# Kernel optimization log

Hardware: AMD Instinct MI355X
Metric: run time of the kernel (lower is better)

Reference implementation:

```python
import jax, jax.numpy as jnp
import numpy as np

B, S, H = 2, 1024, 4096
NH, NKV, HD = 32, 8, 128
THETA = 500000.0
EPS = 1e-6


def _ste(x, q):
    # straight-through estimator: forward q, gradient of identity
    return x + jax.lax.stop_gradient(q - x)


def weight_quant(w):
    # BitNet b1.58 ternary weight quantization (per-tensor mean-abs scale)
    scale = 1.0 / jnp.clip(jnp.mean(jnp.abs(w)), 1e-5)
    wq = jnp.clip(jnp.round(w * scale), -1.0, 1.0) / scale
    return _ste(w, wq)


def act_quant(x):
    # per-token int8 absmax activation quantization
    scale = 127.0 / jnp.clip(jnp.max(jnp.abs(x), axis=-1, keepdims=True), 1e-5)
    xq = jnp.clip(jnp.round(x * scale), -128.0, 127.0) / scale
    return _ste(x, xq)


def bitlinear(x, w):
    # torch Linear convention: w is (out, in)
    return act_quant(x) @ weight_quant(w).T


def rmsnorm(x, w):
    return x * jax.lax.rsqrt(jnp.mean(x * x, axis=-1, keepdims=True) + EPS) * w


def rope(x, cos, sin):
    # x: (b, s, h, hd); pairs are interleaved (even, odd) like view_as_complex
    x2 = x.reshape(*x.shape[:-1], HD // 2, 2)
    a, b = x2[..., 0], x2[..., 1]
    c = cos[None, :, None, :]
    s = sin[None, :, None, :]
    out = jnp.stack([a * c - b * s, a * s + b * c], axis=-1)
    return out.reshape(x.shape)


def setup_inputs() -> dict:
    key = jax.random.key(0)
    ks = jax.random.split(key, 6)
    hidden_states = jax.random.normal(ks[0], (B, S, H), dtype=jnp.float32)
    causal = jnp.tril(jnp.ones((S, S), dtype=bool))
    attention_mask = jnp.where(causal, 0.0, -1e9).astype(jnp.float32)[None, None]
    w_q = jax.random.normal(ks[1], (NH * HD, H), dtype=jnp.float32) * 0.02
    w_k = jax.random.normal(ks[2], (NKV * HD, H), dtype=jnp.float32) * 0.02
    w_v = jax.random.normal(ks[3], (NKV * HD, H), dtype=jnp.float32) * 0.02
    w_o = jax.random.normal(ks[4], (H, NH * HD), dtype=jnp.float32) * 0.02
    subln_w = jnp.ones((NH * HD,), dtype=jnp.float32)
    return {"hidden_states": hidden_states, "attention_mask": attention_mask,
            "w_q": w_q, "w_k": w_k, "w_v": w_v, "w_o": w_o, "subln_w": subln_w}


def reference(hidden_states, attention_mask, w_q, w_k, w_v, w_o, subln_w):
    b, s, _ = hidden_states.shape
    # RoPE tables (precomputed buffer in torch, constant here)
    inv_freq = 1.0 / (THETA ** (jnp.arange(0, HD, 2, dtype=jnp.float32) / HD))
    freqs = jnp.arange(s, dtype=jnp.float32)[:, None] * inv_freq[None, :]  # (s, hd/2)
    cos, sin = jnp.cos(freqs), jnp.sin(freqs)

    q = bitlinear(hidden_states, w_q).reshape(b, s, NH, HD)
    k = bitlinear(hidden_states, w_k).reshape(b, s, NKV, HD)
    v = bitlinear(hidden_states, w_v).reshape(b, s, NKV, HD)

    q = rope(q, cos, sin)
    k = rope(k, cos, sin)

    # GQA: repeat kv heads
    n_rep = NH // NKV
    k = jnp.repeat(k, n_rep, axis=2)  # (b, s, NH, hd)
    v = jnp.repeat(v, n_rep, axis=2)

    scale = 1.0 / np.sqrt(HD)
    scores = jnp.einsum('bqhd,bkhd->bhqk', q, k) * scale
    scores = scores + attention_mask
    attn = jax.nn.softmax(scores.astype(jnp.float32), axis=-1).astype(q.dtype)
    out = jnp.einsum('bhqk,bkhd->bqhd', attn, v).reshape(b, s, NH * HD)

    out = rmsnorm(out, subln_w)  # SubLN before output projection
    out = bitlinear(out, w_o)
    return out
```

## Files before the change

### kernel.cpp

```cpp
#include <hip/hip_runtime.h>
#include <hip/hip_bf16.h>
#include <cstdint>

typedef unsigned short u16;
typedef __bf16 bf16x8 __attribute__((ext_vector_type(8)));
typedef float f32x4 __attribute__((ext_vector_type(4)));
typedef int i32x4 __attribute__((ext_vector_type(4)));

#define SEQ 1024
#define HID 4096
#define NHQ 32
#define NKVH 8
#define HDIM 128
#define NB 2
#define NROWS (NB*SEQ)

static __device__ __forceinline__ u16 f2bf(float x) {
  __hip_bfloat16 h = __float2bfloat16(x);
  return *reinterpret_cast<u16*>(&h);
}

static __device__ __forceinline__ void gload16(const void* g, void* l) {
  __builtin_amdgcn_global_load_lds((__attribute__((address_space(1))) void*)(void*)g,
                                   (__attribute__((address_space(3))) void*)l, 16, 0, 0);
}

static __device__ __forceinline__ int pack4i8(float a, float b, float c, float d,
                                              float s, float lo, float hi) {
  int x0 = (int)fminf(fmaxf(rintf(a*s), lo), hi);
  int x1 = (int)fminf(fmaxf(rintf(b*s), lo), hi);
  int x2 = (int)fminf(fmaxf(rintf(c*s), lo), hi);
  int x3 = (int)fminf(fmaxf(rintf(d*s), lo), hi);
  return (x0 & 255) | ((x1 & 255) << 8) | ((x2 & 255) << 16) | ((x3 & 255) << 24);
}

__global__ __launch_bounds__(256) void k_abssum4(const float* __restrict__ wq_, const float* __restrict__ wk_,
                                                 const float* __restrict__ wv_, const float* __restrict__ wo_,
                                                 float* __restrict__ partial) {
  int bx = blockIdx.x;
  const float* w; long n4; int pbase, lb, nb;
  if (bx < 1024)      { w = wq_; n4 = 4194304; pbase = 0;    lb = bx;        nb = 1024; }
  else if (bx < 1280) { w = wk_; n4 = 1048576; pbase = 1024; lb = bx - 1024; nb = 256; }
  else if (bx < 1536) { w = wv_; n4 = 1048576; pbase = 1280; lb = bx - 1280; nb = 256; }
  else                { w = wo_; n4 = 4194304; pbase = 1536; lb = bx - 1536; nb = 1024; }
  float s = 0.f;
  long stride = (long)nb * 256;
  const float4* w4 = (const float4*)w;
  for (long j = (long)lb*256 + threadIdx.x; j < n4; j += stride) {
    float4 v = w4[j];
    s += fabsf(v.x) + fabsf(v.y) + fabsf(v.z) + fabsf(v.w);
  }
  #pragma unroll
  for (int off = 1; off < 64; off <<= 1) s += __shfl_xor(s, off);
  __shared__ float red[4];
  if ((threadIdx.x & 63) == 0) red[threadIdx.x >> 6] = s;
  __syncthreads();
  if (threadIdx.x == 0) partial[pbase + lb] = red[0] + red[1] + red[2] + red[3];
}

__global__ __launch_bounds__(256) void k_wscale(const float* __restrict__ partial,
                                                float* __restrict__ wsc) {
  __shared__ float red[4];
  const float nelem[4] = {16777216.f, 4194304.f, 4194304.f, 16777216.f};
  const int pbase[4] = {0, 1024, 1280, 1536};
  const int pcnt[4]  = {1024, 256, 256, 1024};
  for (int wi = 0; wi < 4; ++wi) {
    float s = 0.f;
    for (int j = threadIdx.x; j < pcnt[wi]; j += 256) s += partial[pbase[wi] + j];
    #pragma unroll
    for (int off = 1; off < 64; off <<= 1) s += __shfl_xor(s, off);
    if ((threadIdx.x & 63) == 0) red[threadIdx.x >> 6] = s;
    __syncthreads();
    if (threadIdx.x == 0) wsc[wi] = fmaxf((red[0]+red[1]+red[2]+red[3]) / nelem[wi], 1e-5f);
    __syncthreads();
  }
}

__global__ __launch_bounds__(256) void k_quantw8_all(const float* __restrict__ wq_, const float* __restrict__ wk_,
                                                     const float* __restrict__ wv_, const float* __restrict__ wo_,
                                                     char* __restrict__ oq_, char* __restrict__ ok_,
                                                     char* __restrict__ ov_, char* __restrict__ oo_,
                                                     const float* __restrict__ wsc) {
  int bx = blockIdx.x;
  const float* src; char* dst; int idx; long base;
  if (bx < 16384)      { src = wq_; dst = oq_; idx = 0; base = bx; }
  else if (bx < 20480) { src = wk_; dst = ok_; idx = 1; base = bx - 16384; }
  else if (bx < 24576) { src = wv_; dst = ov_; idx = 2; base = bx - 20480; }
  else                 { src = wo_; dst = oo_; idx = 3; base = bx - 24576; }
  long j = base*256 + threadIdx.x;
  long oj = j;
  if (idx <= 1) {
    long row = j >> 10;
    int u = (int)(row & 31);
    long prow = (row & ~31L) | (long)((u >> 1) | ((u & 1) << 4));
    oj = (prow << 10) | (j & 1023);
  }
  float inv = 1.0f / wsc[idx];
  float4 v = ((const float4*)src)[j];
  ((int*)dst)[oj] = pack4i8(v.x, v.y, v.z, v.w, inv, -1.f, 1.f);
}

__global__ __launch_bounds__(256) void k_actq8(const float* __restrict__ x, char* __restrict__ xq,
                                               float* __restrict__ xs) {
  long row = blockIdx.x;
  const float4* xr = (const float4*)(x + row*HID);
  float4 v[4];
  float am = 0.f;
  #pragma unroll
  for (int j = 0; j < 4; ++j) {
    v[j] = xr[j*256 + threadIdx.x];
    am = fmaxf(am, fmaxf(fmaxf(fabsf(v[j].x), fabsf(v[j].y)), fmaxf(fabsf(v[j].z), fabsf(v[j].w))));
  }
  #pragma unroll
  for (int off = 1; off < 64; off <<= 1) am = fmaxf(am, __shfl_xor(am, off));
  __shared__ float red[4];
  if ((threadIdx.x & 63) == 0) red[threadIdx.x >> 6] = am;
  __syncthreads();
  am = fmaxf(fmaxf(red[0], red[1]), fmaxf(red[2], red[3]));
  float amc = fmaxf(am, 1e-5f);
  float s = 127.0f / amc;
  int* oq = (int*)(xq + row*HID);
  #pragma unroll
  for (int j = 0; j < 4; ++j)
    oq[j*256 + threadIdx.x] = pack4i8(v[j].x, v[j].y, v[j].z, v[j].w, s, -128.f, 127.f);
  if (threadIdx.x == 0) xs[row] = amc / 127.0f;
}

__global__ __launch_bounds__(256) void k_gemm8(const char* __restrict__ A, const char* __restrict__ W,
                                               float* __restrict__ C, const float* __restrict__ arow,
                                               const float* __restrict__ wsc, int widx,
                                               int M, int N, int K) {
  __shared__ char As[3][64*64] __attribute__((aligned(16)));
  __shared__ char Ws_[3][128*64] __attribute__((aligned(16)));
  int t = threadIdx.x;
  int bid = blockIdx.x;
  int xcd = bid & 7, w = bid >> 3;
  int bm = ((xcd & 1) << 4) + (w >> 3);
  int bn = ((xcd >> 1) << 3) + (w & 7);
  const char* Ab = A + (long)bm*64*K;
  const char* Wb = W + (long)bn*128*K;
  int lane = t & 63, wid = t >> 6;
  int wr = wid >> 1, wc = wid & 1;
  int lrow = lane & 15, l8 = lane >> 4;
  int xsw = (lrow >> 1) & 3;
  int ch0 = (l8 ^ xsw) * 16;
  i32x4 zero = {0, 0, 0, 0};
  i32x4 acc[2][4];
  #pragma unroll
  for (int mi = 0; mi < 2; ++mi)
    #pragma unroll
    for (int ni = 0; ni < 4; ++ni) acc[mi][ni] = zero;

  int r0 = t >> 2;
  int c0 = ((t & 3) ^ ((t >> 3) & 3)) * 16;
  auto stage = [&](int buf, int kt) {
    gload16(Ab + (long)r0*K + kt*64 + c0, &As[buf][t*16]);
    gload16(Wb + (long)r0*K + kt*64 + c0, &Ws_[buf][t*16]);
    gload16(Wb + (long)(r0+64)*K + kt*64 + c0, &Ws_[buf][(t+256)*16]);
  };

  int nk = K >> 6;
  stage(0, 0); stage(1, 1);
  for (int kt = 0; kt < nk; ++kt) {
    if (kt + 2 < nk) {
      stage((kt + 2) % 3, kt + 2);
      asm volatile("s_waitcnt vmcnt(6)" ::: "memory");
    } else if (kt + 1 < nk) {
      asm volatile("s_waitcnt vmcnt(3)" ::: "memory");
    } else {
      asm volatile("s_waitcnt vmcnt(0)" ::: "memory");
    }
    __builtin_amdgcn_sched_barrier(0);
    __builtin_amdgcn_s_barrier();
    int cur = kt % 3;
    const char* Ac = &As[cur][0];
    const char* Wc = &Ws_[cur][0];
    i32x4 af[2], bfr[4];
    #pragma unroll
    for (int mi = 0; mi < 2; ++mi) af[mi] = *(const i32x4*)&Ac[(wr*32 + mi*16 + lrow)*64 + ch0];
    #pragma unroll
    for (int ni = 0; ni < 4; ++ni) bfr[ni] = *(const i32x4*)&Wc[(wc*64 + ni*16 + lrow)*64 + ch0];
    __builtin_amdgcn_s_setprio(1);
    #pragma unroll
    for (int mi = 0; mi < 2; ++mi)
      #pragma unroll
      for (int ni = 0; ni < 4; ++ni)
        acc[mi][ni] = __builtin_amdgcn_mfma_i32_16x16x64_i8(af[mi], bfr[ni], acc[mi][ni], 0, 0, 0);
    __builtin_amdgcn_s_setprio(0);
    asm volatile("s_waitcnt lgkmcnt(0)" ::: "memory");
    __builtin_amdgcn_sched_barrier(0);
    __builtin_amdgcn_s_barrier();
  }
  float ws = wsc[widx];
  #pragma unroll
  for (int mi = 0; mi < 2; ++mi)
    #pragma unroll
    for (int r = 0; r < 4; ++r) {
      int row = bm*64 + wr*32 + mi*16 + l8*4 + r;
      float sc = arow[row] * ws;
      #pragma unroll
      for (int ni = 0; ni < 4; ++ni) {
        int col = bn*128 + wc*64 + ni*16 + lrow;
        C[(long)row*N + col] = (float)acc[mi][ni][r] * sc;
      }
    }
}

__global__ __launch_bounds__(256) void k_gemm8_qkv(const char* __restrict__ A,
    const char* __restrict__ Wq, const char* __restrict__ Wk, const char* __restrict__ Wv,
    u16* __restrict__ Qb, u16* __restrict__ Kb, u16* __restrict__ Vt,
    const float* __restrict__ arow, const float* __restrict__ wsc,
    const float* __restrict__ cosb, const float* __restrict__ sinb) {
  const int K = 4096;
  int bid = blockIdx.x;
  int xcd = bid & 7, w = bid >> 3;
  int kind, bm, bn;
  const char* W;
  if (w < 64)      { kind = 0; bm = ((xcd & 1) << 3) + (w >> 3); bn = ((xcd >> 1) << 3) + (w & 7); W = Wq; }
  else if (w < 80) { int u = w - 64; kind = 1; bm = (xcd << 1) + (u >> 3); bn = u & 7; W = Wk; }
  else             { int u = w - 80; kind = 2; bm = (xcd << 1) + (u >> 3); bn = u & 7; W = Wv; }

  __shared__ char As[3][128*64] __attribute__((aligned(16)));
  __shared__ char Ws_[3][128*64] __attribute__((aligned(16)));
  int t = threadIdx.x;
  const char* Ab = A + (long)bm*128*K;
  const char* Wb = W + (long)bn*128*K;
  int lane = t & 63, wid = t >> 6;
  int wr = wid >> 1, wc = wid & 1;
  int lrow = lane & 15, l8 = lane >> 4;
  int xsw = (lrow >> 1) & 3;
  int ch0 = (l8 ^ xsw) * 16;
  i32x4 zero = {0, 0, 0, 0};
  i32x4 acc[4][4];
  #pragma unroll
  for (int mi = 0; mi < 4; ++mi)
    #pragma unroll
    for (int ni = 0; ni < 4; ++ni) acc[mi][ni] = zero;

  int f0 = t, f1 = t + 256;
  int r0 = f0 >> 2, c0 = ((f0 & 3) ^ ((f0 >> 3) & 3)) * 16;
  int r1 = f1 >> 2;
  auto stage = [&](int buf, int kt) {
    gload16(Ab + (long)r0*K + kt*64 + c0, &As[buf][f0*16]);
    gload16(Ab + (long)r1*K + kt*64 + c0, &As[buf][f1*16]);
    gload16(Wb + (long)r0*K + kt*64 + c0, &Ws_[buf][f0*16]);
    gload16(Wb + (long)r1*K + kt*64 + c0, &Ws_[buf][f1*16]);
  };

  int nk = K >> 6;
  stage(0, 0); stage(1, 1);
  for (int kt = 0; kt < nk; ++kt) {
    if (kt + 2 < nk) {
      stage((kt + 2) % 3, kt + 2);
      asm volatile("s_waitcnt vmcnt(8)" ::: "memory");
    } else if (kt + 1 < nk) {
      asm volatile("s_waitcnt vmcnt(4)" ::: "memory");
    } else {
      asm volatile("s_waitcnt vmcnt(0)" ::: "memory");
    }
    __builtin_amdgcn_sched_barrier(0);
    __builtin_amdgcn_s_barrier();
    int cur = kt % 3;
    const char* Ac = &As[cur][0];
    const char* Wc = &Ws_[cur][0];
    i32x4 af[4], bfr[4];
    #pragma unroll
    for (int mi = 0; mi < 4; ++mi) af[mi] = *(const i32x4*)&Ac[(wr*64 + mi*16 + lrow)*64 + ch0];
    #pragma unroll
    for (int ni = 0; ni < 4; ++ni) bfr[ni] = *(const i32x4*)&Wc[(wc*64 + ni*16 + lrow)*64 + ch0];
    __builtin_amdgcn_s_setprio(1);
    #pragma unroll
    for (int mi = 0; mi < 4; ++mi)
      #pragma unroll
      for (int ni = 0; ni < 4; ++ni)
        acc[mi][ni] = __builtin_amdgcn_mfma_i32_16x16x64_i8(af[mi], bfr[ni], acc[mi][ni], 0, 0, 0);
    __builtin_amdgcn_s_setprio(0);
    asm volatile("s_waitcnt lgkmcnt(0)" ::: "memory");
    __builtin_amdgcn_sched_barrier(0);
    __builtin_amdgcn_s_barrier();
  }

  if (kind == 2) {
    float ws = wsc[2];
    #pragma unroll
    for (int mi = 0; mi < 4; ++mi) {
      int row0 = bm*128 + wr*64 + mi*16 + l8*4;
      int bidx = row0 >> 10, s0 = row0 & 1023;
      #pragma unroll
      for (int ni = 0; ni < 4; ++ni) {
        int col = bn*128 + wc*64 + ni*16 + lrow;
        int hkv = col >> 7, d = col & 127;
        ushort4 o4;
        o4.x = f2bf((float)acc[mi][ni][0] * arow[row0+0] * ws);
        o4.y = f2bf((float)acc[mi][ni][1] * arow[row0+1] * ws);
        o4.z = f2bf((float)acc[mi][ni][2] * arow[row0+2] * ws);
        o4.w = f2bf((float)acc[mi][ni][3] * arow[row0+3] * ws);
        *(ushort4*)&Vt[(((long)bidx*NKVH + hkv)*HDIM + d)*SEQ + s0] = o4;
      }
    }
  } else {
    float ws = wsc[kind];
    u16* dst = kind ? Kb : Qb;
    int nh = kind ? NKVH : NHQ;
    #pragma unroll
    for (int mi = 0; mi < 4; ++mi) {
      #pragma unroll
      for (int r = 0; r < 4; ++r) {
        int row = bm*128 + wr*64 + mi*16 + l8*4 + r;
        int bidx = row >> 10, s = row & 1023;
        float sc = arow[row] * ws;
        #pragma unroll
        for (int j = 0; j < 2; ++j) {
          float a  = (float)acc[mi][2*j][r] * sc;
          float b2 = (float)acc[mi][2*j+1][r] * sc;
          int B = bn*128 + wc*64 + j*32;
          int h = B >> 7;
          int d = (B & 127) + 2*lrow;
          int i = d >> 1;
          float cc = cosb[(s << 6) + i], sn = sinb[(s << 6) + i];
          ushort2 o2;
          o2.x = f2bf(a*cc - b2*sn);
          o2.y = f2bf(a*sn + b2*cc);
          *(ushort2*)&dst[(((long)bidx*nh + h)*SEQ + s)*HDIM + d] = o2;
        }
      }
    }
  }
}

__global__ __launch_bounds__(256) void k_ropetab(float* __restrict__ cosb, float* __restrict__ sinb) {
  int idx = blockIdx.x*256 + threadIdx.x;
  int s = idx >> 6, i = idx & 63;
  float e = (2.0f * (float)i) / 128.0f;
  float inv = 1.0f / powf(500000.0f, e);
  float f = (float)s * inv;
  cosb[idx] = cosf(f);
  sinb[idx] = sinf(f);
}

__global__ __launch_bounds__(256) void k_attn(const u16* __restrict__ qb, const u16* __restrict__ kb,
                                              const u16* __restrict__ vt, float* __restrict__ ao) {
  int p = blockIdx.x, h = blockIdx.y, b = blockIdx.z;
  int t = threadIdx.x, lane = t & 63, wid = t >> 6;
  int lrow = lane & 15, l8 = lane >> 4;
  int x7 = lrow & 7;

  __shared__ u16 Ks[2][64*128] __attribute__((aligned(16)));
  __shared__ u16 Vs[2][128*64] __attribute__((aligned(16)));
  __shared__ u16 Ps[4][16][72] __attribute__((aligned(16)));

  const u16* kp = kb + ((long)(b*NKVH + (h >> 2)))*SEQ*HDIM;
  const u16* vp = vt + ((long)(b*NKVH + (h >> 2)))*HDIM*SEQ;

  auto stageK = [&](int buf, int j) {
    const u16* src = kp + (long)j*64*HDIM;
    #pragma unroll
    for (int i = 0; i < 4; ++i) {
      int r0 = wid*16 + i*4;
      int row = r0 + (lane >> 4);
      int cg = (lane & 15) ^ (row & 7);
      gload16(src + (long)row*HDIM + cg*8, &Ks[buf][r0*HDIM]);
    }
  };
  auto stageV = [&](int buf, int j) {
    #pragma unroll
    for (int i = 0; i < 4; ++i) {
      int r0 = wid*32 + i*8;
      int row = r0 + (lane >> 3);
      int cg = (lane & 7) ^ (row & 7);
      gload16(vp + (long)row*SEQ + j*64 + cg*8, &Vs[buf][r0*64]);
    }
  };

  for (int phase = 0; phase < 2; ++phase) {
    int qt = phase ? (15 - p) : p;
    int q0 = qt*64 + wid*16;
    const u16* qp = qb + (((long)(b*NHQ + h))*SEQ + q0)*HDIM;
    bf16x8 qf[4];
    #pragma unroll
    for (int ks = 0; ks < 4; ++ks) qf[ks] = *(const bf16x8*)&qp[lrow*HDIM + ks*32 + l8*8];
    f32x4 zero = {0.f, 0.f, 0.f, 0.f};
    f32x4 o[8];
    #pragma unroll
    for (int f = 0; f < 8; ++f) o[f] = zero;
    float m[4], ll[4];
    #pragma unroll
    for (int r = 0; r < 4; ++r) { m[r] = -1e30f; ll[r] = 0.f; }

    int nj = qt + 1;
    stageK(0, 0); stageV(0, 0);
    __syncthreads();
    int cur = 0;
    for (int j = 0; j < nj; ++j) {
      if (j + 1 < nj) { stageK(cur ^ 1, j + 1); stageV(cur ^ 1, j + 1); }
      const u16* Kc = Ks[cur];
      const u16* Vc = Vs[cur];
      f32x4 sc4[4];
      #pragma unroll
      for (int ni = 0; ni < 4; ++ni) sc4[ni] = zero;
      __builtin_amdgcn_s_setprio(1);
      #pragma unroll
      for (int ni = 0; ni < 4; ++ni) {
        int row = ni*16 + lrow;
        #pragma unroll
        for (int ks = 0; ks < 4; ++ks) {
          int cl = (ks*4 + l8) ^ x7;
          bf16x8 kfr = *(const bf16x8*)&Kc[row*HDIM + cl*8];
          sc4[ni] = __builtin_amdgcn_mfma_f32_16x16x32_bf16(qf[ks], kfr, sc4[ni], 0, 0, 0);
        }
      }
      __builtin_amdgcn_s_setprio(0);
      const float scale = 0.08838834764831845f;
      float pm[4] = {-1e30f, -1e30f, -1e30f, -1e30f};
      float pv[4][4];
      bool diag = (j == qt);
      #pragma unroll
      for (int ni = 0; ni < 4; ++ni) {
        int kv = j*64 + ni*16 + lrow;
        #pragma unroll
        for (int r = 0; r < 4; ++r) {
          int qr = q0 + l8*4 + r;
          float val = sc4[ni][r] * scale;
          if (diag && kv > qr) val = -1e30f;
          pv[ni][r] = val;
          pm[r] = fmaxf(pm[r], val);
        }
      }
      #pragma unroll
      for (int r = 0; r < 4; ++r) {
        #pragma unroll
        for (int off = 1; off < 16; off <<= 1) pm[r] = fmaxf(pm[r], __shfl_xor(pm[r], off));
      }
      float fr[4], rs[4];
      #pragma unroll
      for (int r = 0; r < 4; ++r) {
        float nm = fmaxf(m[r], pm[r]);
        fr[r] = __expf(m[r] - nm);
        m[r] = nm; rs[r] = 0.f;
      }
      #pragma unroll
      for (int ni = 0; ni < 4; ++ni)
        #pragma unroll
        for (int r = 0; r < 4; ++r) {
          float pe = __expf(pv[ni][r] - m[r]);
          pv[ni][r] = pe; rs[r] += pe;
        }
      #pragma unroll
      for (int r = 0; r < 4; ++r) {
        #pragma unroll
        for (int off = 1; off < 16; off <<= 1) rs[r] += __shfl_xor(rs[r], off);
        ll[r] = ll[r]*fr[r] + rs[r];
      }
      #pragma unroll
      for (int f = 0; f < 8; ++f) {
        o[f][0] *= fr[0]; o[f][1] *= fr[1]; o[f][2] *= fr[2]; o[f][3] *= fr[3];
      }
      #pragma unroll
      for (int ni = 0; ni < 4; ++ni)
        #pragma unroll
        for (int r = 0; r < 4; ++r)
          Ps[wid][l8*4 + r][ni*16 + lrow] = f2bf(pv[ni][r]);
      bf16x8 pf0 = *(const bf16x8*)&Ps[wid][lrow][l8*8];
      bf16x8 pf1 = *(const bf16x8*)&Ps[wid][lrow][32 + l8*8];
      __builtin_amdgcn_s_setprio(1);
      #pragma unroll
      for (int f = 0; f < 8; ++f) {
        int d = f*16 + lrow;
        bf16x8 v0 = *(const bf16x8*)&Vc[d*64 + ((l8) ^ x7)*8];
        bf16x8 v1 = *(const bf16x8*)&Vc[d*64 + ((4 + l8) ^ x7)*8];
        o[f] = __builtin_amdgcn_mfma_f32_16x16x32_bf16(pf0, v0, o[f], 0, 0, 0);
        o[f] = __builtin_amdgcn_mfma_f32_16x16x32_bf16(pf1, v1, o[f], 0, 0, 0);
      }
      __builtin_amdgcn_s_setprio(0);
      __syncthreads();
      cur ^= 1;
    }
    float invl[4];
    #pragma unroll
    for (int r = 0; r < 4; ++r) invl[r] = 1.0f / ll[r];
    #pragma unroll
    for (int f = 0; f < 8; ++f)
      #pragma unroll
      for (int r = 0; r < 4; ++r) {
        long row = (long)b*SEQ + q0 + l8*4 + r;
        ao[row*HID + h*HDIM + f*16 + lrow] = o[f][r] * invl[r];
      }
    __syncthreads();
  }
}

__global__ __launch_bounds__(256) void k_rmsq8(const float* __restrict__ x, const float* __restrict__ w,
                                               char* __restrict__ yq, float* __restrict__ ys) {
  long row = blockIdx.x;
  const float4* xr = (const float4*)(x + row*HID);
  const float4* wr = (const float4*)w;
  float4 v[4];
  float ss = 0.f;
  #pragma unroll
  for (int j = 0; j < 4; ++j) {
    v[j] = xr[j*256 + threadIdx.x];
    ss += v[j].x*v[j].x + v[j].y*v[j].y + v[j].z*v[j].z + v[j].w*v[j].w;
  }
  #pragma unroll
  for (int off = 1; off < 64; off <<= 1) ss += __shfl_xor(ss, off);
  __shared__ float red[4];
  if ((threadIdx.x & 63) == 0) red[threadIdx.x >> 6] = ss;
  __syncthreads();
  ss = red[0] + red[1] + red[2] + red[3];
  __syncthreads();
  float rn = rsqrtf(ss / (float)HID + 1e-6f);
  float4 y[4];
  float am = 0.f;
  #pragma unroll
  for (int j = 0; j < 4; ++j) {
    float4 wv = wr[j*256 + threadIdx.x];
    y[j].x = v[j].x * rn * wv.x; y[j].y = v[j].y * rn * wv.y;
    y[j].z = v[j].z * rn * wv.z; y[j].w = v[j].w * rn * wv.w;
    am = fmaxf(am, fmaxf(fmaxf(fabsf(y[j].x), fabsf(y[j].y)), fmaxf(fabsf(y[j].z), fabsf(y[j].w))));
  }
  #pragma unroll
  for (int off = 1; off < 64; off <<= 1) am = fmaxf(am, __shfl_xor(am, off));
  if ((threadIdx.x & 63) == 0) red[threadIdx.x >> 6] = am;
  __syncthreads();
  am = fmaxf(fmaxf(red[0], red[1]), fmaxf(red[2], red[3]));
  float amc = fmaxf(am, 1e-5f);
  float s = 127.0f / amc;
  int* oq = (int*)(yq + row*HID);
  #pragma unroll
  for (int j = 0; j < 4; ++j)
    oq[j*256 + threadIdx.x] = pack4i8(y[j].x, y[j].y, y[j].z, y[j].w, s, -128.f, 127.f);
  if (threadIdx.x == 0) ys[row] = amc / 127.0f;
}

extern "C" void kernel_launch(void* const* d_in, const int* in_sizes, int n_in,
                              void* d_out, int out_size, void* d_ws, size_t ws_size,
                              hipStream_t stream) {
  const float* hs    = (const float*)d_in[0];
  const float* w_q   = (const float*)d_in[2];
  const float* w_k   = (const float*)d_in[3];
  const float* w_v   = (const float*)d_in[4];
  const float* w_o   = (const float*)d_in[5];
  const float* subln = (const float*)d_in[6];

  char* ws = (char*)d_ws;
  char*  wqq = (char*)(ws + 0L);
  char*  wqk = (char*)(ws + 16777216L);
  char*  wqv = (char*)(ws + 20971520L);
  char*  wqo = (char*)(ws + 25165824L);
  char*  xq  = (char*)(ws + 41943040L);
  float* ao  = (float*)(ws + 50331648L);
  char*  yq  = (char*)(ws + 83886080L);
  u16*   qb  = (u16*)(ws + 92274688L);
  u16*   kb  = (u16*)(ws + 109051904L);
  u16*   vtb = (u16*)(ws + 113246208L);
  float* cosb= (float*)(ws + 117440512L);
  float* sinb= (float*)(ws + 117702656L);
  float* xs  = (float*)(ws + 117964800L);
  float* ys  = (float*)(ws + 117972992L);
  float* wsc = (float*)(ws + 117981184L);
  float* par = (float*)(ws + 117981248L);
  float* out = (float*)d_out;

  k_abssum4<<<2560, 256, 0, stream>>>(w_q, w_k, w_v, w_o, par);
  k_wscale<<<1, 256, 0, stream>>>(par, wsc);

  k_quantw8_all<<<40960, 256, 0, stream>>>(w_q, w_k, w_v, w_o, wqq, wqk, wqv, wqo, wsc);
  k_ropetab<<<256, 256, 0, stream>>>(cosb, sinb);
  k_actq8<<<NROWS, 256, 0, stream>>>(hs, xq, xs);

  k_gemm8_qkv<<<768, 256, 0, stream>>>(xq, wqq, wqk, wqv, qb, kb, vtb, xs, wsc, cosb, sinb);

  k_attn<<<dim3(8, 32, 2), 256, 0, stream>>>(qb, kb, vtb, ao);

  k_rmsq8<<<NROWS, 256, 0, stream>>>(ao, subln, yq, ys);

  k_gemm8<<<1024, 256, 0, stream>>>(yq, wqo, out, ys, wsc, 3, NROWS, 4096, 4096);
}
```

Before: 277.0 us.

## Use two-wave 128x128 int8 GEMM tiles with one barrier per k-step

Both int8 GEMMs now run 128-thread blocks where each wave computes a 64x128 output tile (4x8 MFMAs), raising register-level reuse of the LDS fragments. The output-projection GEMM grows from 64x128 to 128x128 tiles, halving its grid. The k-loop is restructured: fragments are read from LDS first, the next global-to-LDS stage is issued afterwards, and only one barrier per iteration remains. The cost is more accumulator registers per thread, fewer blocks, and a tighter ordering between the LDS reads and overwriting the triple buffer.

```diff
diff --git a/kernel.cpp b/kernel.cpp
--- a/kernel.cpp
+++ b/kernel.cpp
@@ -126,87 +126,85 @@
   if (threadIdx.x == 0) xs[row] = amc / 127.0f;
 }
 
-__global__ __launch_bounds__(256) void k_gemm8(const char* __restrict__ A, const char* __restrict__ W,
-                                               float* __restrict__ C, const float* __restrict__ arow,
-                                               const float* __restrict__ wsc, int widx,
-                                               int M, int N, int K) {
-  __shared__ char As[3][64*64] __attribute__((aligned(16)));
+__global__ __launch_bounds__(128, 2) void k_gemm8(const char* __restrict__ A, const char* __restrict__ W,
+                                                  float* __restrict__ C, const float* __restrict__ arow,
+                                                  const float* __restrict__ wsc, int widx,
+                                                  int M, int N, int K) {
+  __shared__ char As[3][128*64] __attribute__((aligned(16)));
   __shared__ char Ws_[3][128*64] __attribute__((aligned(16)));
   int t = threadIdx.x;
   int bid = blockIdx.x;
   int xcd = bid & 7, w = bid >> 3;
-  int bm = ((xcd & 1) << 4) + (w >> 3);
+  int bm = ((xcd & 1) << 3) + (w >> 3);
   int bn = ((xcd >> 1) << 3) + (w & 7);
-  const char* Ab = A + (long)bm*64*K;
+  const char* Ab = A + (long)bm*128*K;
   const char* Wb = W + (long)bn*128*K;
   int lane = t & 63, wid = t >> 6;
-  int wr = wid >> 1, wc = wid & 1;
   int lrow = lane & 15, l8 = lane >> 4;
-  int xsw = (lrow >> 1) & 3;
-  int ch0 = (l8 ^ xsw) * 16;
+  int ch0 = (l8 ^ ((lrow >> 1) & 3)) * 16;
   i32x4 zero = {0, 0, 0, 0};
-  i32x4 acc[2][4];
-  #pragma unroll
-  for (int mi = 0; mi < 2; ++mi)
-    #pragma unroll
-    for (int ni = 0; ni < 4; ++ni) acc[mi][ni] = zero;
-
-  int r0 = t >> 2;
-  int c0 = ((t & 3) ^ ((t >> 3) & 3)) * 16;
+  i32x4 acc[4][8];
+  #pragma unroll
+  for (int mi = 0; mi < 4; ++mi)
+    #pragma unroll
+    for (int ni = 0; ni < 8; ++ni) acc[mi][ni] = zero;
+
   auto stage = [&](int buf, int kt) {
-    gload16(Ab + (long)r0*K + kt*64 + c0, &As[buf][t*16]);
-    gload16(Wb + (long)r0*K + kt*64 + c0, &Ws_[buf][t*16]);
-    gload16(Wb + (long)(r0+64)*K + kt*64 + c0, &Ws_[buf][(t+256)*16]);
+    #pragma unroll
+    for (int i = 0; i < 4; ++i) {
+      int c = t + 128*i;
+      int row = c >> 2;
+      int ci = ((c & 3) ^ ((row >> 1) & 3)) * 16;
+      gload16(Ab + (long)row*K + kt*64 + ci, &As[buf][c*16]);
+      gload16(Wb + (long)row*K + kt*64 + ci, &Ws_[buf][c*16]);
+    }
   };
 
   int nk = K >> 6;
   stage(0, 0); stage(1, 1);
+  asm volatile("s_waitcnt vmcnt(8)" ::: "memory");
+  __builtin_amdgcn_sched_barrier(0);
+  __builtin_amdgcn_s_barrier();
+  __builtin_amdgcn_sched_barrier(0);
   for (int kt = 0; kt < nk; ++kt) {
-    if (kt + 2 < nk) {
-      stage((kt + 2) % 3, kt + 2);
-      asm volatile("s_waitcnt vmcnt(6)" ::: "memory");
-    } else if (kt + 1 < nk) {
-      asm volatile("s_waitcnt vmcnt(3)" ::: "memory");
-    } else {
-      asm volatile("s_waitcnt vmcnt(0)" ::: "memory");
-    }
-    __builtin_amdgcn_sched_barrier(0);
-    __builtin_amdgcn_s_barrier();
     int cur = kt % 3;
-    const char* Ac = &As[cur][0];
-    const char* Wc = &Ws_[cur][0];
-    i32x4 af[2], bfr[4];
-    #pragma unroll
-    for (int mi = 0; mi < 2; ++mi) af[mi] = *(const i32x4*)&Ac[(wr*32 + mi*16 + lrow)*64 + ch0];
-    #pragma unroll
-    for (int ni = 0; ni < 4; ++ni) bfr[ni] = *(const i32x4*)&Wc[(wc*64 + ni*16 + lrow)*64 + ch0];
+    i32x4 af[4], bfr[8];
+    #pragma unroll
+    for (int mi = 0; mi < 4; ++mi) af[mi] = *(const i32x4*)&As[cur][(wid*64 + mi*16 + lrow)*64 + ch0];
+    #pragma unroll
+    for (int ni = 0; ni < 8; ++ni) bfr[ni] = *(const i32x4*)&Ws_[cur][(ni*16 + lrow)*64 + ch0];
+    if (kt + 2 < nk) stage((kt + 2) % 3, kt + 2);
     __builtin_amdgcn_s_setprio(1);
     #pragma unroll
-    for (int mi = 0; mi < 2; ++mi)
-      #pragma unroll
-      for (int ni = 0; ni < 4; ++ni)
+    for (int mi = 0; mi < 4; ++mi)
+      #pragma unroll
+      for (int ni = 0; ni < 8; ++ni)
         acc[mi][ni] = __builtin_amdgcn_mfma_i32_16x16x64_i8(af[mi], bfr[ni], acc[mi][ni], 0, 0, 0);
     __builtin_amdgcn_s_setprio(0);
-    asm volatile("s_waitcnt lgkmcnt(0)" ::: "memory");
-    __builtin_amdgcn_sched_barrier(0);
-    __builtin_amdgcn_s_barrier();
+    if (kt + 2 < nk)      asm volatile("s_waitcnt vmcnt(8)" ::: "memory");
+    else if (kt + 1 < nk) asm volatile("s_waitcnt vmcnt(0)" ::: "memory");
+    if (kt + 1 < nk) {
+      __builtin_amdgcn_sched_barrier(0);
+      __builtin_amdgcn_s_barrier();
+      __builtin_amdgcn_sched_barrier(0);
+    }
   }
   float ws = wsc[widx];
   #pragma unroll
-  for (int mi = 0; mi < 2; ++mi)
+  for (int mi = 0; mi < 4; ++mi)
     #pragma unroll
     for (int r = 0; r < 4; ++r) {
-      int row = bm*64 + wr*32 + mi*16 + l8*4 + r;
+      int row = bm*128 + wid*64 + mi*16 + l8*4 + r;
       float sc = arow[row] * ws;
       #pragma unroll
-      for (int ni = 0; ni < 4; ++ni) {
-        int col = bn*128 + wc*64 + ni*16 + lrow;
+      for (int ni = 0; ni < 8; ++ni) {
+        int col = bn*128 + ni*16 + lrow;
         C[(long)row*N + col] = (float)acc[mi][ni][r] * sc;
       }
     }
 }
 
-__global__ __launch_bounds__(256) void k_gemm8_qkv(const char* __restrict__ A,
+__global__ __launch_bounds__(128, 2) void k_gemm8_qkv(const char* __restrict__ A,
     const char* __restrict__ Wq, const char* __restrict__ Wk, const char* __restrict__ Wv,
     u16* __restrict__ Qb, u16* __restrict__ Kb, u16* __restrict__ Vt,
     const float* __restrict__ arow, const float* __restrict__ wsc,
@@ -226,69 +224,65 @@
   const char* Ab = A + (long)bm*128*K;
   const char* Wb = W + (long)bn*128*K;
   int lane = t & 63, wid = t >> 6;
-  int wr = wid >> 1, wc = wid & 1;
   int lrow = lane & 15, l8 = lane >> 4;
-  int xsw = (lrow >> 1) & 3;
-  int ch0 = (l8 ^ xsw) * 16;
+  int ch0 = (l8 ^ ((lrow >> 1) & 3)) * 16;
   i32x4 zero = {0, 0, 0, 0};
-  i32x4 acc[4][4];
+  i32x4 acc[4][8];
   #pragma unroll
   for (int mi = 0; mi < 4; ++mi)
     #pragma unroll
-    for (int ni = 0; ni < 4; ++ni) acc[mi][ni] = zero;
-
-  int f0 = t, f1 = t + 256;
-  int r0 = f0 >> 2, c0 = ((f0 & 3) ^ ((f0 >> 3) & 3)) * 16;
-  int r1 = f1 >> 2;
+    for (int ni = 0; ni < 8; ++ni) acc[mi][ni] = zero;
+
   auto stage = [&](int buf, int kt) {
-    gload16(Ab + (long)r0*K + kt*64 + c0, &As[buf][f0*16]);
-    gload16(Ab + (long)r1*K + kt*64 + c0, &As[buf][f1*16]);
-    gload16(Wb + (long)r0*K + kt*64 + c0, &Ws_[buf][f0*16]);
-    gload16(Wb + (long)r1*K + kt*64 + c0, &Ws_[buf][f1*16]);
+    #pragma unroll
+    for (int i = 0; i < 4; ++i) {
+      int c = t + 128*i;
+      int row = c >> 2;
+      int ci = ((c & 3) ^ ((row >> 1) & 3)) * 16;
+      gload16(Ab + (long)row*K + kt*64 + ci, &As[buf][c*16]);
+      gload16(Wb + (long)row*K + kt*64 + ci, &Ws_[buf][c*16]);
+    }
   };
 
   int nk = K >> 6;
   stage(0, 0); stage(1, 1);
+  asm volatile("s_waitcnt vmcnt(8)" ::: "memory");
+  __builtin_amdgcn_sched_barrier(0);
+  __builtin_amdgcn_s_barrier();
+  __builtin_amdgcn_sched_barrier(0);
   for (int kt = 0; kt < nk; ++kt) {
-    if (kt + 2 < nk) {
-      stage((kt + 2) % 3, kt + 2);
-      asm volatile("s_waitcnt vmcnt(8)" ::: "memory");
-    } else if (kt + 1 < nk) {
-      asm volatile("s_waitcnt vmcnt(4)" ::: "memory");
-    } else {
-      asm volatile("s_waitcnt vmcnt(0)" ::: "memory");
-    }
-    __builtin_amdgcn_sched_barrier(0);
-    __builtin_amdgcn_s_barrier();
     int cur = kt % 3;
-    const char* Ac = &As[cur][0];
-    const char* Wc = &Ws_[cur][0];
-    i32x4 af[4], bfr[4];
-    #pragma unroll
-    for (int mi = 0; mi < 4; ++mi) af[mi] = *(const i32x4*)&Ac[(wr*64 + mi*16 + lrow)*64 + ch0];
-    #pragma unroll
-    for (int ni = 0; ni < 4; ++ni) bfr[ni] = *(const i32x4*)&Wc[(wc*64 + ni*16 + lrow)*64 + ch0];
+    i32x4 af[4], bfr[8];
+    #pragma unroll
+    for (int mi = 0; mi < 4; ++mi) af[mi] = *(const i32x4*)&As[cur][(wid*64 + mi*16 + lrow)*64 + ch0];
+    #pragma unroll
+    for (int ni = 0; ni < 8; ++ni) bfr[ni] = *(const i32x4*)&Ws_[cur][(ni*16 + lrow)*64 + ch0];
+    if (kt + 2 < nk) stage((kt + 2) % 3, kt + 2);
     __builtin_amdgcn_s_setprio(1);
     #pragma unroll
     for (int mi = 0; mi < 4; ++mi)
       #pragma unroll
-      for (int ni = 0; ni < 4; ++ni)
+      for (int ni = 0; ni < 8; ++ni)
         acc[mi][ni] = __builtin_amdgcn_mfma_i32_16x16x64_i8(af[mi], bfr[ni], acc[mi][ni], 0, 0, 0);
     __builtin_amdgcn_s_setprio(0);
-    asm volatile("s_waitcnt lgkmcnt(0)" ::: "memory");
-    __builtin_amdgcn_sched_barrier(0);
-    __builtin_amdgcn_s_barrier();
+    if (kt + 2 < nk)      asm volatile("s_waitcnt vmcnt(8)" ::: "memory");
+    else if (kt + 1 < nk) asm volatile("s_waitcnt vmcnt(0)" ::: "memory");
+    if (kt + 1 < nk) {
+      __builtin_amdgcn_sched_barrier(0);
+      __builtin_amdgcn_s_barrier();
+      __builtin_amdgcn_sched_barrier(0);
+    }
   }
 
   if (kind == 2) {
     float ws = wsc[2];
     #pragma unroll
     for (int mi = 0; mi < 4; ++mi) {
-      int row0 = bm*128 + wr*64 + mi*16 + l8*4;
+      int row0 = bm*128 + wid*64 + mi*16 + l8*4;
       int bidx = row0 >> 10, s0 = row0 & 1023;
       #pragma unroll
-      for (int ni = 0; ni < 4; ++ni) {
-        int col = bn*128 + wc*64 + ni*16 + lrow;
+      for (int ni = 0; ni < 8; ++ni) {
+        int col = bn*128 + ni*16 + lrow;
         int hkv = col >> 7, d = col & 127;
         ushort4 o4;
         o4.x = f2bf((float)acc[mi][ni][0] * arow[row0+0] * ws);
@@ -306,14 +300,14 @@
     for (int mi = 0; mi < 4; ++mi) {
       #pragma unroll
       for (int r = 0; r < 4; ++r) {
-        int row = bm*128 + wr*64 + mi*16 + l8*4 + r;
+        int row = bm*128 + wid*64 + mi*16 + l8*4 + r;
         int bidx = row >> 10, s = row & 1023;
         float sc = arow[row] * ws;
         #pragma unroll
-        for (int j = 0; j < 2; ++j) {
+        for (int j = 0; j < 4; ++j) {
           float a  = (float)acc[mi][2*j][r] * sc;
           float b2 = (float)acc[mi][2*j+1][r] * sc;
-          int B = bn*128 + wc*64 + j*32;
+          int B = bn*128 + j*32;
           int h = B >> 7;
           int d = (B & 127) + 2*lrow;
           int i = d >> 1;
@@ -568,11 +562,11 @@
   k_ropetab<<<256, 256, 0, stream>>>(cosb, sinb);
   k_actq8<<<NROWS, 256, 0, stream>>>(hs, xq, xs);
 
-  k_gemm8_qkv<<<768, 256, 0, stream>>>(xq, wqq, wqk, wqv, qb, kb, vtb, xs, wsc, cosb, sinb);
+  k_gemm8_qkv<<<768, 128, 0, stream>>>(xq, wqq, wqk, wqv, qb, kb, vtb, xs, wsc, cosb, sinb);
 
   k_attn<<<dim3(8, 32, 2), 256, 0, stream>>>(qb, kb, vtb, ao);
 
   k_rmsq8<<<NROWS, 256, 0, stream>>>(ao, subln, yq, ys);
 
-  k_gemm8<<<1024, 256, 0, stream>>>(yq, wqo, out, ys, wsc, 3, NROWS, 4096, 4096);
-}
+  k_gemm8<<<512, 128, 0, stream>>>(yq, wqo, out, ys, wsc, 3, NROWS, 4096, 4096);
+}
```

After: 245.9 us, median of 2. 11.2% less time.
